# Performance work log

Measured on AMD Instinct MI355X. Metric: run time of the kernel, lower is better.

## Reference

```python
import jax, jax.numpy as jnp
import numpy as np

N = 8192
FEAT = 256
HID = 64
ALPHA = 0.2  # leaky relu slope
NEG = -9e15


def setup_inputs() -> dict:
    key = jax.random.key(0)
    k1, k2, k3, k4, k5 = jax.random.split(key, 5)
    inputs = jax.random.normal(k1, (N, FEAT), dtype=jnp.float32)
    adj = jax.random.randint(k2, (N, N), 0, 2, dtype=jnp.int32)
    tree_attention = jax.random.uniform(k3, (N, N), dtype=jnp.float32)
    # xavier_uniform with gain=1.414
    def xavier(k, shape, gain=1.414):
        fan_in, fan_out = shape[0], shape[1]
        bound = gain * np.sqrt(6.0 / (fan_in + fan_out))
        return jax.random.uniform(k, shape, jnp.float32, -bound, bound)
    W = xavier(k4, (FEAT, HID))
    a = xavier(k5, (2 * HID, 1))
    return {"inputs": inputs, "adj": adj, "tree_attention": tree_attention,
            "W": W, "a": a}


def reference(inputs, adj, tree_attention, W, a):
    # h: [N, HID]
    h = inputs @ W
    # e_ij = leakyrelu(h_i . a[:HID] + h_j . a[HID:])  -- decomposed form of
    # the repeat/cat a_input construction, same math without the O(N^2*2H) tensor.
    s_src = h @ a[:HID]          # [N, 1]
    s_dst = h @ a[HID:]          # [N, 1]
    e = jax.nn.leaky_relu(s_src + s_dst.T, negative_slope=ALPHA)  # [N, N]
    attention = jnp.where(adj > 0, e, jnp.float32(NEG))
    attention = jax.nn.softmax(attention, axis=1)
    # dropout is identity in eval; controlFlag=False skips beta/gama mix
    h_prime = attention @ h      # [N, HID]
    return jax.nn.relu(h_prime)  # concat=True
```

## Files before the change

### kernel.cpp

```cpp
#include <hip/hip_runtime.h>
#include <stdint.h>

#define N 8192
#define FEAT 256
#define HID 64
#define ALPHA 0.2f
#define SBOUND 16.0f
#define LOG2E 1.44269504088896f

typedef __attribute__((ext_vector_type(8))) short short8;
typedef __attribute__((ext_vector_type(4))) float floatx4;

static __device__ __forceinline__ unsigned short f32_to_bf16(float f) {
    union { float f; unsigned int u; } c; c.f = f;
    unsigned int u = c.u;
    unsigned int r = u + 0x7FFFu + ((u >> 16) & 1u);
    return (unsigned short)(r >> 16);
}

__global__ __launch_bounds__(256) void k1_prep(
    const float* __restrict__ inputs, const float* __restrict__ W,
    const float* __restrict__ a,
    float* __restrict__ s_src, float* __restrict__ s_dst,
    unsigned short* __restrict__ hfrag, float* __restrict__ acc_zero)
{
    __shared__ float inlds[16 * FEAT];
    const int t = threadIdx.x;
    const int rb = blockIdx.x * 16;

    {
        const int totf4 = (N * HID + N) / 4;
        float4 z = make_float4(0.f, 0.f, 0.f, 0.f);
        for (int i = blockIdx.x * 256 + t; i < totf4; i += gridDim.x * 256)
            ((float4*)acc_zero)[i] = z;
    }

    {
        const float4* in4 = (const float4*)(inputs + (size_t)rb * FEAT);
        float4* il4 = (float4*)inlds;
        for (int i = t; i < 16 * FEAT / 4; i += 256) il4[i] = in4[i];
    }
    __syncthreads();

    const int d = t & 63;
    const int wv = t >> 6;
    const float asrc = a[d];
    const float adst = a[HID + d];

    float h0 = 0.f, h1 = 0.f, h2 = 0.f, h3 = 0.f;
    const float* wp = W + d;
    const float* ip = inlds + (wv * 4) * FEAT;
    #pragma unroll 4
    for (int k = 0; k < FEAT; ++k) {
        float wk = wp[(size_t)k * HID];
        h0 = fmaf(ip[k],            wk, h0);
        h1 = fmaf(ip[FEAT + k],     wk, h1);
        h2 = fmaf(ip[2 * FEAT + k], wk, h2);
        h3 = fmaf(ip[3 * FEAT + k], wk, h3);
    }

    float hv[4] = {h0, h1, h2, h3};
    #pragma unroll
    for (int rr = 0; rr < 4; ++rr) {
        const int row = rb + wv * 4 + rr;
        float vs = hv[rr] * asrc;
        float vd = hv[rr] * adst;
        #pragma unroll
        for (int mm = 32; mm >= 1; mm >>= 1) {
            vs += __shfl_xor(vs, mm, 64);
            vd += __shfl_xor(vd, mm, 64);
        }
        if (d == 0) { s_src[row] = vs; s_dst[row] = vd; }

        unsigned short hb = f32_to_bf16(hv[rr]);
        const int ks = row >> 5, kk = row & 31, quad = kk >> 3, v = kk & 7;
        const int td = d >> 4, n = d & 15;
        const int lane_ = quad * 16 + n;
        hfrag[(size_t)(((ks * 4 + td) * 64 + lane_) * 8 + v)] = hb;
    }
}

__global__ __launch_bounds__(256, 4) void k2_main(
    const int* __restrict__ adj,
    const float* __restrict__ s_src, const float* __restrict__ s_dst,
    const unsigned short* __restrict__ hfrag,
    float* __restrict__ acc_g, float* __restrict__ l_acc)
{
    __shared__ float comb[4 * 16 * HID];
    __shared__ float lcomb[4 * 16];

    const int t = threadIdx.x;
    const int lane = t & 63, wave = t >> 6;
    const int rowgroup = blockIdx.x >> 1, jblock = blockIdx.x & 1;
    const int rb = rowgroup * 16;
    const int jbase = (jblock * 4 + wave) * 1024;
    const int m = lane & 15, quad = lane >> 4;
    const int row = rb + m;

    const float ssrc = s_src[row];
    const float mt = ssrc + SBOUND;
    const float mi = fmaxf(mt, 0.f) + ALPHA * fminf(mt, 0.f);
    const float mi2 = mi * LOG2E;

    const int4*   adjp = (const int4*)(adj + (size_t)row * N + jbase + quad * 8);
    const float4* sdp  = (const float4*)(s_dst + jbase + quad * 8);
    const short8* bp   = (const short8*)hfrag;
    const int ks0 = jbase >> 5;

    floatx4 acc[4];
    #pragma unroll
    for (int td = 0; td < 4; ++td) acc[td] = (floatx4){0.f, 0.f, 0.f, 0.f};
    float lsum = 0.f;

    for (int s = 0; s < 32; ++s) {
        int4   aj0 = adjp[s * 8];
        int4   aj1 = adjp[s * 8 + 1];
        float4 sd0 = sdp[s * 8];
        float4 sd1 = sdp[s * 8 + 1];
        const int ks = ks0 + s;
        short8 B0 = bp[(ks * 4 + 0) * 64 + lane];
        short8 B1 = bp[(ks * 4 + 1) * 64 + lane];
        short8 B2 = bp[(ks * 4 + 2) * 64 + lane];
        short8 B3 = bp[(ks * 4 + 3) * 64 + lane];

        const float sdv[8] = {sd0.x, sd0.y, sd0.z, sd0.w, sd1.x, sd1.y, sd1.z, sd1.w};
        const int   ajv[8] = {aj0.x, aj0.y, aj0.z, aj0.w, aj1.x, aj1.y, aj1.z, aj1.w};
        short8 A;
        #pragma unroll
        for (int v = 0; v < 8; ++v) {
            float tt = ssrc + sdv[v];
            float lr = fmaf(ALPHA, fminf(tt, 0.f), fmaxf(tt, 0.f));
            float p  = __builtin_amdgcn_exp2f(fmaf(lr, LOG2E, -mi2));
            p = (ajv[v] > 0) ? p : 0.f;
            lsum += p;
            A[v] = (short)f32_to_bf16(p);
        }
        acc[0] = __builtin_amdgcn_mfma_f32_16x16x32_bf16(A, B0, acc[0], 0, 0, 0);
        acc[1] = __builtin_amdgcn_mfma_f32_16x16x32_bf16(A, B1, acc[1], 0, 0, 0);
        acc[2] = __builtin_amdgcn_mfma_f32_16x16x32_bf16(A, B2, acc[2], 0, 0, 0);
        acc[3] = __builtin_amdgcn_mfma_f32_16x16x32_bf16(A, B3, acc[3], 0, 0, 0);
    }

    const int n_ = lane & 15;
    #pragma unroll
    for (int td = 0; td < 4; ++td)
        #pragma unroll
        for (int reg = 0; reg < 4; ++reg) {
            int il = quad * 4 + reg;
            comb[wave * (16 * HID) + il * HID + td * 16 + n_] = acc[td][reg];
        }
    float ls = lsum;
    ls += __shfl_xor(ls, 16, 64);
    ls += __shfl_xor(ls, 32, 64);
    if (lane < 16) lcomb[wave * 16 + lane] = ls;
    __syncthreads();

    for (int f = t; f < 16 * HID; f += 256) {
        float sv = comb[f] + comb[f + 1024] + comb[f + 2048] + comb[f + 3072];
        int il = f >> 6, dd = f & 63;
        atomicAdd(&acc_g[(size_t)(rb + il) * HID + dd], sv);
    }
    if (t < 16) {
        float lv = lcomb[t] + lcomb[16 + t] + lcomb[32 + t] + lcomb[48 + t];
        atomicAdd(&l_acc[rb + t], lv);
    }
}

__global__ __launch_bounds__(256) void k3_final(
    const float* __restrict__ acc_g, const float* __restrict__ l_acc,
    float* __restrict__ out)
{
    const int idx = blockIdx.x * 256 + threadIdx.x;
    float4 v = ((const float4*)acc_g)[idx];
    const int i = (idx * 4) >> 6;
    float li = l_acc[i];
    float inv = (li > 0.f) ? 1.0f / li : 0.f;
    float4 o;
    o.x = fmaxf(v.x * inv, 0.f);
    o.y = fmaxf(v.y * inv, 0.f);
    o.z = fmaxf(v.z * inv, 0.f);
    o.w = fmaxf(v.w * inv, 0.f);
    ((float4*)out)[idx] = o;
}

extern "C" void kernel_launch(void* const* d_in, const int* in_sizes, int n_in,
                              void* d_out, int out_size, void* d_ws, size_t ws_size,
                              hipStream_t stream) {
    const float* inputs = (const float*)d_in[0];
    const int*   adj    = (const int*)d_in[1];
    const float* W      = (const float*)d_in[3];
    const float* a      = (const float*)d_in[4];
    float* out = (float*)d_out;

    float* acc_g = (float*)d_ws;
    float* l_acc = acc_g + (size_t)N * HID;
    float* s_src = l_acc + N;
    float* s_dst = s_src + N;
    unsigned short* hfrag = (unsigned short*)(s_dst + N);

    k1_prep<<<512, 256, 0, stream>>>(inputs, W, a, s_src, s_dst, hfrag, acc_g);
    k2_main<<<1024, 256, 0, stream>>>(adj, s_src, s_dst, hfrag, acc_g, l_acc);
    k3_final<<<512, 256, 0, stream>>>(acc_g, l_acc, out);
}
```

Baseline: 533.2 us.

## Factor exp of leaky-relu into per-column precomputed exponentials and prefetch adj

Precomputes exp(s_dst) and exp(alpha*s_dst) per column in the prep kernel. The main loop then forms each attention weight as a select plus a multiply by a per-row constant, with no per-element exp or leaky-relu. It also software-prefetches the next adjacency tile, disables loop unrolling, and simplifies the bf16 rounding to round-half-up. This trades transcendental work for two extra column vectors read per tile, and it can overflow or lose precision when s_dst is large.

```diff
diff --git a/kernel.cpp b/kernel.cpp
--- a/kernel.cpp
+++ b/kernel.cpp
@@ -13,15 +13,14 @@
 
 static __device__ __forceinline__ unsigned short f32_to_bf16(float f) {
     union { float f; unsigned int u; } c; c.f = f;
-    unsigned int u = c.u;
-    unsigned int r = u + 0x7FFFu + ((u >> 16) & 1u);
-    return (unsigned short)(r >> 16);
+    return (unsigned short)((c.u + 0x8000u) >> 16);
 }
 
 __global__ __launch_bounds__(256) void k1_prep(
     const float* __restrict__ inputs, const float* __restrict__ W,
     const float* __restrict__ a,
     float* __restrict__ s_src, float* __restrict__ s_dst,
+    float* __restrict__ e1, float* __restrict__ e2,
     unsigned short* __restrict__ hfrag, float* __restrict__ acc_zero)
 {
     __shared__ float inlds[16 * FEAT];
@@ -70,7 +69,12 @@
             vs += __shfl_xor(vs, mm, 64);
             vd += __shfl_xor(vd, mm, 64);
         }
-        if (d == 0) { s_src[row] = vs; s_dst[row] = vd; }
+        if (d == 0) {
+            s_src[row] = vs;
+            s_dst[row] = vd;
+            e1[row] = __builtin_amdgcn_exp2f(vd * LOG2E);
+            e2[row] = __builtin_amdgcn_exp2f(ALPHA * vd * LOG2E);
+        }
 
         unsigned short hb = f32_to_bf16(hv[rr]);
         const int ks = row >> 5, kk = row & 31, quad = kk >> 3, v = kk & 7;
@@ -82,7 +86,8 @@
 
 __global__ __launch_bounds__(256, 4) void k2_main(
     const int* __restrict__ adj,
-    const float* __restrict__ s_src, const float* __restrict__ s_dst,
+    const float* __restrict__ s_src,
+    const float* __restrict__ e1, const float* __restrict__ e2,
     const unsigned short* __restrict__ hfrag,
     float* __restrict__ acc_g, float* __restrict__ l_acc)
 {
@@ -100,10 +105,13 @@
     const float ssrc = s_src[row];
     const float mt = ssrc + SBOUND;
     const float mi = fmaxf(mt, 0.f) + ALPHA * fminf(mt, 0.f);
-    const float mi2 = mi * LOG2E;
+    const float c1 = __builtin_amdgcn_exp2f((ssrc - mi) * LOG2E);
+    const float c2 = __builtin_amdgcn_exp2f((ALPHA * ssrc - mi) * LOG2E);
+    const float thrE = __builtin_amdgcn_exp2f(-ssrc * LOG2E);
 
     const int4*   adjp = (const int4*)(adj + (size_t)row * N + jbase + quad * 8);
-    const float4* sdp  = (const float4*)(s_dst + jbase + quad * 8);
+    const float4* e1p  = (const float4*)(e1 + jbase + quad * 8);
+    const float4* e2p  = (const float4*)(e2 + jbase + quad * 8);
     const short8* bp   = (const short8*)hfrag;
     const int ks0 = jbase >> 5;
 
@@ -112,25 +120,33 @@
     for (int td = 0; td < 4; ++td) acc[td] = (floatx4){0.f, 0.f, 0.f, 0.f};
     float lsum = 0.f;
 
+    int4 naj0 = adjp[0];
+    int4 naj1 = adjp[1];
+
+    #pragma clang loop unroll(disable)
     for (int s = 0; s < 32; ++s) {
-        int4   aj0 = adjp[s * 8];
-        int4   aj1 = adjp[s * 8 + 1];
-        float4 sd0 = sdp[s * 8];
-        float4 sd1 = sdp[s * 8 + 1];
+        const int4 aj0 = naj0, aj1 = naj1;
+        const int sn = (s < 31) ? s + 1 : 31;
+        naj0 = adjp[sn * 8];
+        naj1 = adjp[sn * 8 + 1];
+        float4 e1a = e1p[s * 8], e1b = e1p[s * 8 + 1];
+        float4 e2a = e2p[s * 8], e2b = e2p[s * 8 + 1];
         const int ks = ks0 + s;
         short8 B0 = bp[(ks * 4 + 0) * 64 + lane];
         short8 B1 = bp[(ks * 4 + 1) * 64 + lane];
         short8 B2 = bp[(ks * 4 + 2) * 64 + lane];
         short8 B3 = bp[(ks * 4 + 3) * 64 + lane];
 
-        const float sdv[8] = {sd0.x, sd0.y, sd0.z, sd0.w, sd1.x, sd1.y, sd1.z, sd1.w};
+        const float e1v[8] = {e1a.x, e1a.y, e1a.z, e1a.w, e1b.x, e1b.y, e1b.z, e1b.w};
+        const float e2v[8] = {e2a.x, e2a.y, e2a.z, e2a.w, e2b.x, e2b.y, e2b.z, e2b.w};
         const int   ajv[8] = {aj0.x, aj0.y, aj0.z, aj0.w, aj1.x, aj1.y, aj1.z, aj1.w};
         short8 A;
         #pragma unroll
         for (int v = 0; v < 8; ++v) {
-            float tt = ssrc + sdv[v];
-            float lr = fmaf(ALPHA, fminf(tt, 0.f), fmaxf(tt, 0.f));
-            float p  = __builtin_amdgcn_exp2f(fmaf(lr, LOG2E, -mi2));
+            const bool pos = e1v[v] > thrE;
+            float f = pos ? e1v[v] : e2v[v];
+            float c = pos ? c1 : c2;
+            float p = f * c;
             p = (ajv[v] > 0) ? p : 0.f;
             lsum += p;
             A[v] = (short)f32_to_bf16(p);
@@ -197,8 +213,10 @@
     float* s_src = l_acc + N;
     float* s_dst = s_src + N;
     unsigned short* hfrag = (unsigned short*)(s_dst + N);
-
-    k1_prep<<<512, 256, 0, stream>>>(inputs, W, a, s_src, s_dst, hfrag, acc_g);
-    k2_main<<<1024, 256, 0, stream>>>(adj, s_src, s_dst, hfrag, acc_g, l_acc);
+    float* e1 = (float*)(hfrag + (size_t)N * HID);
+    float* e2 = e1 + N;
+
+    k1_prep<<<512, 256, 0, stream>>>(inputs, W, a, s_src, s_dst, e1, e2, hfrag, acc_g);
+    k2_main<<<1024, 256, 0, stream>>>(adj, s_src, e1, e2, hfrag, acc_g, l_acc);
     k3_final<<<512, 256, 0, stream>>>(acc_g, l_acc, out);
 }
```

Result: no change. 531.9 us (-0.2%).
